# Kernel tuning notes

Measured on AMD Instinct MI355X. Metric: run time of the kernel, lower is better.

Reference implementation:

```python
import jax, jax.numpy as jnp
import numpy as np
import math

V, TB, C, H, L = 50257, 1024, 1024, 16, 8
B, T = 2, 1024
D = C // H


def setup_inputs() -> dict:
    key = jax.random.key(0)
    ks = jax.random.split(key, 16)
    s = 0.02
    n = lambda k, shp: (jax.random.normal(k, shp, jnp.float32) * s)
    inp = {
        "idx": jax.random.randint(ks[0], (B, T), 0, V),
        "tok_emb": n(ks[1], (V, C)),
        "pos_emb": n(ks[2], (1, TB, C)),
        # per-layer stacked params (torch Linear convention: W is [out, in])
        "Wq": n(ks[3], (L, C, C)), "bq": jnp.zeros((L, C)),
        "Wk": n(ks[4], (L, C, C)), "bk": jnp.zeros((L, C)),
        "Wv": n(ks[5], (L, C, C)), "bv": jnp.zeros((L, C)),
        "Wp": n(ks[6], (L, C, C)), "bp": jnp.zeros((L, C)),
        "ln1_w": jnp.ones((L, C)), "ln1_b": jnp.zeros((L, C)),
        "ln2_w": jnp.ones((L, C)), "ln2_b": jnp.zeros((L, C)),
        "W1": n(ks[7], (L, 4 * C, C)), "b1": jnp.zeros((L, 4 * C)),
        "W2": n(ks[8], (L, C, 4 * C)), "b2": jnp.zeros((L, C)),
        "lnf_w": jnp.ones((C,)), "lnf_b": jnp.zeros((C,)),
        "head_w": n(ks[9], (V, C)),
    }
    return inp


def _layer_norm(x, w, b, eps=1e-5):
    mu = x.mean(-1, keepdims=True)
    var = x.var(-1, keepdims=True)
    return (x - mu) * jax.lax.rsqrt(var + eps) * w + b


def _gpt_forward(idx, tok_emb, pos_emb, Wq, bq, Wk, bk, Wv, bv, Wp, bp,
                 ln1_w, ln1_b, ln2_w, ln2_b, W1, b1, W2, b2, lnf_w, lnf_b, head_w):
    b, t = idx.shape
    x = tok_emb[idx] + pos_emb[:, :t, :]  # [B, T, C]; drop = identity (eval)
    causal = jnp.tril(jnp.ones((t, t), dtype=bool))  # [T, T]
    scale = 1.0 / math.sqrt(D)

    def block(x, p):
        (wq, bq_, wk, bk_, wv, bv_, wp, bp_, l1w, l1b, l2w, l2b, w1, b1_, w2, b2_) = p
        h = _layer_norm(x, l1w, l1b)
        q = (h @ wq.T + bq_).reshape(b, t, H, D).transpose(0, 2, 1, 3)  # [B,H,T,D]
        k = (h @ wk.T + bk_).reshape(b, t, H, D).transpose(0, 2, 1, 3)
        v = (h @ wv.T + bv_).reshape(b, t, H, D).transpose(0, 2, 1, 3)
        att = jnp.einsum("bhqd,bhkd->bhqk", q, k) * scale
        att = jnp.where(causal, att, -jnp.inf)
        att = jax.nn.softmax(att, axis=-1)
        y = jnp.einsum("bhqk,bhkd->bhqd", att, v)
        y = y.transpose(0, 2, 1, 3).reshape(b, t, C)
        x = x + (y @ wp.T + bp_)
        h2 = _layer_norm(x, l2w, l2b)
        m = jax.nn.gelu(h2 @ w1.T + b1_, approximate=False)  # torch nn.GELU (erf)
        x = x + (m @ w2.T + b2_)
        return x, None

    params = (Wq, bq, Wk, bk, Wv, bv, Wp, bp, ln1_w, ln1_b, ln2_w, ln2_b, W1, b1, W2, b2)
    x, _ = jax.lax.scan(block, x, params)
    x = _layer_norm(x, lnf_w, lnf_b)
    logits = x @ head_w.T  # [B, T, V]
    return logits


def reference(idx, tok_emb, pos_emb, Wq, bq, Wk, bk, Wv, bv, Wp, bp,
              ln1_w, ln1_b, ln2_w, ln2_b, W1, b1, W2, b2, lnf_w, lnf_b, head_w):
    return _gpt_forward(idx, tok_emb, pos_emb, Wq, bq, Wk, bk, Wv, bv, Wp, bp,
                        ln1_w, ln1_b, ln2_w, ln2_b, W1, b1, W2, b2, lnf_w, lnf_b, head_w)
```

## Files before the change

kernel.cpp:

```cpp
#include <hip/hip_runtime.h>
#include <math.h>

#define V_ 50257
#define C_ 1024
#define H_ 16
#define L_ 8
#define B_ 2
#define T_ 1024
#define BT_ 2048
#define CC_ (C_*C_)
#define QLD_ 3072

typedef unsigned short ushort_t;
using bf16x8 = __attribute__((ext_vector_type(8))) short;
using f32x4  = __attribute__((ext_vector_type(4))) float;

#define AS1 __attribute__((address_space(1)))
#define AS3 __attribute__((address_space(3)))
#define VMCNT0() asm volatile("s_waitcnt vmcnt(0)" ::: "memory")
#define LGKM0()  asm volatile("s_waitcnt lgkmcnt(0)" ::: "memory")
#define RBAR()   asm volatile("s_barrier" ::: "memory")

__device__ __forceinline__ ushort_t f2bf(float f){
  union { float f; unsigned u; } a; a.f = f;
  unsigned r = a.u + 0x7fffu + ((a.u >> 16) & 1u);
  return (ushort_t)(r >> 16);
}

__device__ __forceinline__ unsigned cvtpk_bf16(float a, float b){
  unsigned r;
  asm("v_cvt_pk_bf16_f32 %0, %1, %2" : "=v"(r) : "v"(a), "v"(b));
  return r;
}

__device__ __forceinline__ float wave_sum(float v){
  #pragma unroll
  for(int o=32;o>0;o>>=1) v += __shfl_down(v,o,64);
  return v;
}

__global__ __launch_bounds__(256) void cvt_blk(const float* __restrict__ s, ushort_t* __restrict__ d,
    long inner4, int nblk, long dstStride4){
  long total = inner4 * nblk;
  for(long i = (long)blockIdx.x*256 + threadIdx.x; i < total; i += (long)gridDim.x*256){
    long blk = i / inner4, r = i - blk*inner4;
    float4 v = ((const float4*)s)[i];
    ushort4 o; o.x=f2bf(v.x); o.y=f2bf(v.y); o.z=f2bf(v.z); o.w=f2bf(v.w);
    ((ushort4*)d)[blk*dstStride4 + r] = o;
  }
}

__global__ __launch_bounds__(256) void cvt_qkv(const float* __restrict__ wq,
    const float* __restrict__ wk, const float* __restrict__ wv, ushort_t* __restrict__ d){
  const long inner4 = (long)CC_/4;
  const long total = (long)L_*3*inner4;
  for(long i = (long)blockIdx.x*256 + threadIdx.x; i < total; i += (long)gridDim.x*256){
    long l = i / (3*inner4), r = i - l*3*inner4;
    int which = (int)(r / inner4);
    long rr = r - (long)which*inner4;
    const float* s = (which==0 ? wq : which==1 ? wk : wv) + (l*inner4 + rr)*4;
    float4 v = *(const float4*)s;
    ushort4 o; o.x=f2bf(v.x); o.y=f2bf(v.y); o.z=f2bf(v.z); o.w=f2bf(v.w);
    ((ushort4*)d)[i] = o;
  }
}

__global__ __launch_bounds__(256) void pack_qkv_bias(const float* __restrict__ bq,
    const float* __restrict__ bk, const float* __restrict__ bv, float* __restrict__ dst){
  int i = blockIdx.x*256 + threadIdx.x;
  int l = i / QLD_, c = i - l*QLD_;
  float v;
  if(c < C_)            v = bq[l*C_ + c];
  else if(c < 2*C_)     v = bk[l*C_ + c - C_];
  else                  v = bv[l*C_ + c - 2*C_];
  dst[i] = v;
}

__global__ __launch_bounds__(256) void embed_kernel(const int* __restrict__ idx,
    const float* __restrict__ tok, const float* __restrict__ pos, float* __restrict__ x){
  int i = blockIdx.x*256 + threadIdx.x;
  int c = i & (C_-1); int bt = i >> 10; int t = bt & (T_-1);
  x[i] = tok[(size_t)idx[bt]*C_ + c] + pos[t*C_ + c];
}

__global__ __launch_bounds__(256) void ln_kernel(const float* in, const float* __restrict__ w,
    const float* __restrict__ b, float* outF, ushort_t* outB){
  int row = blockIdx.x;
  const float* xr = in + (size_t)row*C_;
  float vals[4]; float sum=0.f, sq=0.f;
  #pragma unroll
  for(int l=0;l<4;l++){ float v = xr[threadIdx.x + l*256]; vals[l]=v; sum+=v; sq+=v*v; }
  __shared__ float r1[4], r2[4];
  float s1 = wave_sum(sum), s2 = wave_sum(sq);
  int wid = threadIdx.x>>6, lane = threadIdx.x&63;
  if(lane==0){ r1[wid]=s1; r2[wid]=s2; }
  __syncthreads();
  float tot  = r1[0]+r1[1]+r1[2]+r1[3];
  float tot2 = r2[0]+r2[1]+r2[2]+r2[3];
  float mu  = tot * (1.f/C_);
  float var = tot2 * (1.f/C_) - mu*mu;
  float inv = rsqrtf(var + 1e-5f);
  #pragma unroll
  for(int l=0;l<4;l++){
    int c = threadIdx.x + l*256;
    float v = (vals[l]-mu)*inv*w[c] + b[c];
    if(outB) outB[(size_t)row*C_ + c] = f2bf(v);
    else     outF[(size_t)row*C_ + c] = v;
  }
}

template<int BN>
__global__ __launch_bounds__(256) void gemm_mfma(
    const ushort_t* __restrict__ A, const ushort_t* __restrict__ W,
    const float* __restrict__ bias, const float* resid,
    float* outF, ushort_t* outB,
    int M, int N, int K, int act, int nt, int qs)
{
  constexpr int BM = 128;
  constexpr int NSB = BN/16;
  constexpr int NBF = BN/32;
  __shared__ __align__(16) short sA[3][8*512];
  __shared__ __align__(16) short sB[3][NSB*512];
  const int tid  = threadIdx.x;
  const int lane = tid & 63, wid = tid >> 6;
  const int wr = wid >> 1, wc = wid & 1;
  const int nwg = gridDim.x * gridDim.y;
  const int lid = blockIdx.x + gridDim.x * blockIdx.y;
  const int swz = (lid & 7) * (nwg >> 3) + (lid >> 3);
  const int m0 = (swz % gridDim.x) * BM, n0 = (swz / gridDim.x) * BN;
  const int r16 = lane & 15, kq = lane >> 4;

  auto stage = [&](int buf, int k0){
    #pragma unroll
    for(int s2=0; s2<2; ++s2){
      int s = wid*2 + s2;
      const ushort_t* g = A + (size_t)(m0 + s*16 + r16)*K + k0 + kq*8;
      __builtin_amdgcn_global_load_lds((const AS1 void*)g,
          (AS3 void*)&sA[buf][s*512], 16, 0, 0);
    }
    #pragma unroll
    for(int s2=0; s2<NSB/4; ++s2){
      int s = wid*(NSB/4) + s2;
      int gn = n0 + s*16 + r16; if(gn >= N) gn = N-1;
      const ushort_t* g = W + (size_t)gn*K + k0 + kq*8;
      __builtin_amdgcn_global_load_lds((const AS1 void*)g,
          (AS3 void*)&sB[buf][s*512], 16, 0, 0);
    }
  };

  f32x4 acc[4][NBF];
  #pragma unroll
  for(int i=0;i<4;i++)
    #pragma unroll
    for(int j=0;j<NBF;j++) acc[i][j] = (f32x4){0.f,0.f,0.f,0.f};

  const int NT = K >> 5;
  stage(0, 0); stage(1, 32); stage(2, 64);

  int cur = 0;
  for(int t=0; t<NT; ++t){
    if(t+2 < NT){
      if constexpr(BN==128) asm volatile("s_waitcnt vmcnt(8)" ::: "memory");
      else                  asm volatile("s_waitcnt vmcnt(6)" ::: "memory");
    } else if(t+1 < NT){
      if constexpr(BN==128) asm volatile("s_waitcnt vmcnt(4)" ::: "memory");
      else                  asm volatile("s_waitcnt vmcnt(3)" ::: "memory");
    } else {
      VMCNT0();
    }
    RBAR();
    bf16x8 af[4], bfr[NBF];
    #pragma unroll
    for(int m=0;m<4;m++) af[m] = *(const bf16x8*)&sA[cur][(wr*4+m)*512 + lane*8];
    #pragma unroll
    for(int n=0;n<NBF;n++) bfr[n] = *(const bf16x8*)&sB[cur][(wc*NBF+n)*512 + lane*8];
    LGKM0();
    RBAR();
    if(t+3 < NT) stage(cur, (t+3)*32);
    #pragma unroll
    for(int m=0;m<4;m++)
      #pragma unroll
      for(int n=0;n<NBF;n++)
        acc[m][n] = __builtin_amdgcn_mfma_f32_16x16x32_bf16(af[m], bfr[n], acc[m][n], 0, 0, 0);
    cur = (cur==2) ? 0 : cur+1;
  }

  const int colb = n0 + wc*(BN/2);
  #pragma unroll
  for(int m=0;m<4;m++){
    int rowb = m0 + wr*64 + m*16 + kq*4;
    #pragma unroll
    for(int n=0;n<NBF;n++){
      int col = colb + n*16 + r16;
      if(col >= N) continue;
      float bv = bias ? bias[col] : 0.f;
      #pragma unroll
      for(int i=0;i<4;i++){
        int row = rowb + i;
        float v = acc[m][n][i] + bv;
        if(qs && col < C_) v *= 0.125f;
        if(act) v = 0.5f*v*(1.f + erff(v*0.70710678118654752f));
        if(resid) v += resid[(size_t)row*N + col];
        if(outB) outB[(size_t)row*N + col] = f2bf(v);
        else if(nt) __builtin_nontemporal_store(v, &outF[(size_t)row*N + col]);
        else outF[(size_t)row*N + col] = v;
      }
    }
  }
}

template<int BN>
__global__ __launch_bounds__(256) void gemm_s64(
    const ushort_t* __restrict__ A, const ushort_t* __restrict__ W,
    const float* __restrict__ bias, const float* resid,
    float* outF, ushort_t* outB,
    int M, int N, int K, int act, int qs)
{
  constexpr int NSB = BN/16;
  constexpr int NBF = BN/32;
  constexpr int LPW = 1 + NSB/4;
  __shared__ __align__(16) short sA[3][4*512];
  __shared__ __align__(16) short sB[3][NSB*512];
  const int tid  = threadIdx.x;
  const int lane = tid & 63, wid = tid >> 6;
  const int wr = wid >> 1, wc = wid & 1;
  const int nwg = gridDim.x * gridDim.y;
  const int lid = blockIdx.x + gridDim.x * blockIdx.y;
  const int swz = (lid & 7) * (nwg >> 3) + (lid >> 3);
  const int m0 = (swz % gridDim.x) * 64, n0 = (swz / gridDim.x) * BN;
  const int r16 = lane & 15, kq = lane >> 4;

  auto stage = [&](int buf, int k0){
    {
      const ushort_t* g = A + (size_t)(m0 + wid*16 + r16)*K + k0 + kq*8;
      __builtin_amdgcn_global_load_lds((const AS1 void*)g,
          (AS3 void*)&sA[buf][wid*512], 16, 0, 0);
    }
    #pragma unroll
    for(int s2=0; s2<NSB/4; ++s2){
      int s = wid*(NSB/4) + s2;
      const ushort_t* g = W + (size_t)(n0 + s*16 + r16)*K + k0 + kq*8;
      __builtin_amdgcn_global_load_lds((const AS1 void*)g,
          (AS3 void*)&sB[buf][s*512], 16, 0, 0);
    }
  };

  f32x4 acc[2][NBF];
  #pragma unroll
  for(int i=0;i<2;i++)
    #pragma unroll
    for(int j=0;j<NBF;j++) acc[i][j] = (f32x4){0.f,0.f,0.f,0.f};

  const int NT = K >> 5;
  stage(0, 0); stage(1, 32); stage(2, 64);

  int cur = 0;
  for(int t=0; t<NT; ++t){
    if(t+2 < NT){
      if constexpr(LPW==2) asm volatile("s_waitcnt vmcnt(4)" ::: "memory");
      else                 asm volatile("s_waitcnt vmcnt(6)" ::: "memory");
    } else if(t+1 < NT){
      if constexpr(LPW==2) asm volatile("s_waitcnt vmcnt(2)" ::: "memory");
      else                 asm volatile("s_waitcnt vmcnt(3)" ::: "memory");
    } else {
      VMCNT0();
    }
    RBAR();
    bf16x8 af[2], bfr[NBF];
    #pragma unroll
    for(int m=0;m<2;m++) af[m] = *(const bf16x8*)&sA[cur][(wr*2+m)*512 + lane*8];
    #pragma unroll
    for(int n=0;n<NBF;n++) bfr[n] = *(const bf16x8*)&sB[cur][(wc*NBF+n)*512 + lane*8];
    LGKM0();
    RBAR();
    if(t+3 < NT) stage(cur, (t+3)*32);
    #pragma unroll
    for(int m=0;m<2;m++)
      #pragma unroll
      for(int n=0;n<NBF;n++)
        acc[m][n] = __builtin_amdgcn_mfma_f32_16x16x32_bf16(af[m], bfr[n], acc[m][n], 0, 0, 0);
    cur = (cur==2) ? 0 : cur+1;
  }

  const int colb = n0 + wc*(BN/2);
  #pragma unroll
  for(int m=0;m<2;m++){
    int rowb = m0 + wr*32 + m*16 + kq*4;
    #pragma unroll
    for(int n=0;n<NBF;n++){
      int col = colb + n*16 + r16;
      float bv = bias ? bias[col] : 0.f;
      #pragma unroll
      for(int i=0;i<4;i++){
        int row = rowb + i;
        float v = acc[m][n][i] + bv;
        if(qs && col < C_) v *= 0.125f;
        if(act) v = 0.5f*v*(1.f + erff(v*0.70710678118654752f));
        if(resid) v += resid[(size_t)row*N + col];
        if(outB) outB[(size_t)row*N + col] = f2bf(v);
        else outF[(size_t)row*N + col] = v;
      }
    }
  }
}

__global__ __launch_bounds__(256) void flash_kernel(const ushort_t* __restrict__ qkv,
    ushort_t* __restrict__ y){
  const int tid = threadIdx.x, lane = tid & 63, wid = tid >> 6;
  const int r16 = lane & 15, kq = lane >> 4;
  const int lid = blockIdx.x + 16*blockIdx.y;
  const int swz = (lid & 7)*64 + (lid >> 3);
  const int qt = 15 - (swz & 15), bh = swz >> 4;
  const int b = bh >> 4, h = bh & 15;
  const int q0 = qt*64, qw0 = q0 + wid*16;
  const int qa = qw0 + r16;

  __shared__ __align__(16) short Kt[2][8][512];
  __shared__ __align__(16) short VT[2][64][72];
  __shared__ __align__(16) short Pl[4][16][72];
  __shared__ __align__(16) short Ol[4][16][72];

  const size_t rowQ = (size_t)(b*T_ + qa)*QLD_ + h*64 + kq*8;
  bf16x8 qf0 = *(const bf16x8*)(qkv + rowQ);
  bf16x8 qf1 = *(const bf16x8*)(qkv + rowQ + 32);

  auto stageK = [&](int buf, int jt){
    #pragma unroll
    for(int s2=0;s2<2;s2++){
      int s = wid*2 + s2;
      const ushort_t* g = qkv + (size_t)(b*T_ + jt*64 + (s>>1)*16 + r16)*QLD_
                          + C_ + h*64 + (s&1)*32 + kq*8;
      __builtin_amdgcn_global_load_lds((const AS1 void*)g,
          (AS3 void*)&Kt[buf][s][lane*8], 16, 0, 0);
    }
  };

  f32x4 acc[4];
  #pragma unroll
  for(int t=0;t<4;t++) acc[t] = (f32x4){0.f,0.f,0.f,0.f};
  float m_r = -INFINITY, l_r = 0.f;

  {
    stageK(0, 0);
    const ushort_t* vg = qkv + (size_t)(b*T_ + lane)*QLD_ + 2*C_ + h*64;
    bf16x8 va = *(const bf16x8*)(vg + wid*8);
    bf16x8 vb = *(const bf16x8*)(vg + 32 + wid*8);
    VMCNT0();
    #pragma unroll
    for(int j=0;j<8;j++){ VT[0][wid*8+j][lane]=va[j]; VT[0][32+wid*8+j][lane]=vb[j]; }
    __syncthreads();
  }

  const int njt = qt + 1;
  for(int jt=0; jt<njt; ++jt){
    const int cur = jt & 1;
    const bool more = (jt+1) < njt;
    bf16x8 vr0, vr1;
    if(more){
      stageK(cur^1, jt+1);
      const ushort_t* vg = qkv + (size_t)(b*T_ + (jt+1)*64 + lane)*QLD_ + 2*C_ + h*64;
      vr0 = *(const bf16x8*)(vg + wid*8);
      vr1 = *(const bf16x8*)(vg + 32 + wid*8);
    }

    f32x4 st[4];
    __builtin_amdgcn_s_setprio(1);
    #pragma unroll
    for(int kr=0;kr<4;kr++){
      st[kr] = (f32x4){0.f,0.f,0.f,0.f};
      st[kr] = __builtin_amdgcn_mfma_f32_16x16x32_bf16(*(const bf16x8*)&Kt[cur][kr*2+0][lane*8], qf0, st[kr], 0,0,0);
      st[kr] = __builtin_amdgcn_mfma_f32_16x16x32_bf16(*(const bf16x8*)&Kt[cur][kr*2+1][lane*8], qf1, st[kr], 0,0,0);
    }
    __builtin_amdgcn_s_setprio(0);

    float vals[16];
    if(jt == njt-1){
      #pragma unroll
      for(int kr=0;kr<4;kr++)
        #pragma unroll
        for(int i=0;i<4;i++){
          int ka = jt*64 + kr*16 + 4*kq + i;
          vals[kr*4+i] = (ka <= qa) ? st[kr][i] : -INFINITY;
        }
    } else {
      #pragma unroll
      for(int kr=0;kr<4;kr++)
        #pragma unroll
        for(int i=0;i<4;i++) vals[kr*4+i] = st[kr][i];
    }
    float t8[8];
    #pragma unroll
    for(int i=0;i<8;i++) t8[i] = fmaxf(vals[i], vals[i+8]);
    float t4a = fmaxf(t8[0],t8[4]), t4b = fmaxf(t8[1],t8[5]);
    float t4c = fmaxf(t8[2],t8[6]), t4d = fmaxf(t8[3],t8[7]);
    float pmax = fmaxf(fmaxf(t4a,t4b), fmaxf(t4c,t4d));
    pmax = fmaxf(pmax, __shfl_xor(pmax, 16, 64));
    pmax = fmaxf(pmax, __shfl_xor(pmax, 32, 64));

    if(!__all(pmax - m_r <= 8.f)){
      float mnew = fmaxf(m_r, pmax);
      float alpha = __expf(m_r - mnew);
      l_r *= alpha;
      #pragma unroll
      for(int t=0;t<4;t++)
        #pragma unroll
        for(int j=0;j<4;j++) acc[t][j] *= alpha;
      m_r = mnew;
    }

    float ps = 0.f;
    #pragma unroll
    for(int kr=0;kr<4;kr++){
      float p0 = __expf(vals[kr*4+0]-m_r), p1 = __expf(vals[kr*4+1]-m_r);
      float p2 = __expf(vals[kr*4+2]-m_r), p3 = __expf(vals[kr*4+3]-m_r);
      ps += (p0+p1)+(p2+p3);
      *(unsigned*)&Pl[wid][r16][kr*16 + 4*kq]     = cvtpk_bf16(p0, p1);
      *(unsigned*)&Pl[wid][r16][kr*16 + 4*kq + 2] = cvtpk_bf16(p2, p3);
    }
    ps += __shfl_xor(ps, 16, 64);
    ps += __shfl_xor(ps, 32, 64);
    l_r += ps;

    union { bf16x8 v8; uint2 u2[2]; } pf, vf;
    __builtin_amdgcn_s_setprio(1);
    #pragma unroll
    for(int ks2=0; ks2<2; ks2++){
      pf.u2[0] = *(const uint2*)&Pl[wid][r16][ks2*32 + kq*8];
      pf.u2[1] = *(const uint2*)&Pl[wid][r16][ks2*32 + kq*8 + 4];
      #pragma unroll
      for(int db=0; db<4; db++){
        vf.u2[0] = *(const uint2*)&VT[cur][16*db + r16][ks2*32 + kq*8];
        vf.u2[1] = *(const uint2*)&VT[cur][16*db + r16][ks2*32 + kq*8 + 4];
        acc[db] = __builtin_amdgcn_mfma_f32_16x16x32_bf16(vf.v8, pf.v8, acc[db], 0,0,0);
      }
    }
    __builtin_amdgcn_s_setprio(0);

    if(more){
      VMCNT0();
      #pragma unroll
      for(int j=0;j<8;j++){ VT[cur^1][wid*8+j][lane]=vr0[j]; VT[cur^1][32+wid*8+j][lane]=vr1[j]; }
    }
    __syncthreads();
  }

  float linv = 1.f / l_r;
  #pragma unroll
  for(int db=0; db<4; db++)
    #pragma unroll
    for(int i=0;i<4;i++)
      Ol[wid][r16][16*db + 4*kq + i] = (short)f2bf(acc[db][i]*linv);
  int q = lane >> 2, c0 = (lane & 3)*16;
  const short* src = &Ol[wid][q][c0];
  uint2 a0 = *(const uint2*)(src+0), a1 = *(const uint2*)(src+4);
  uint2 a2 = *(const uint2*)(src+8), a3 = *(const uint2*)(src+12);
  ushort_t* dst = y + (size_t)(b*T_ + qw0 + q)*C_ + h*64 + c0;
  uint4 w0 = {a0.x, a0.y, a1.x, a1.y}, w1 = {a2.x, a2.y, a3.x, a3.y};
  *(uint4*)(dst+0) = w0;
  *(uint4*)(dst+8) = w1;
}

__global__ __launch_bounds__(256) void gemm_nt(const float* __restrict__ A, const float* __restrict__ W,
    const float* __restrict__ bias, const float* resid, float* Cm,
    int M, int N, int K, int act){
  __shared__ float As[16][68];
  __shared__ float Bs[16][68];
  int m0 = blockIdx.y*64, n0 = blockIdx.x*64;
  int tid = threadIdx.x;
  int tx = tid & 15, ty = tid >> 4;
  float acc[4][4] = {};
  for(int k0=0;k0<K;k0+=16){
    #pragma unroll
    for(int l=0;l<4;l++){
      int li = tid + l*256;
      int r = li >> 4, c = li & 15;
      int gm = m0 + r, gn = n0 + r, gk = k0 + c;
      As[c][r] = (gm<M) ? A[(size_t)gm*K + gk] : 0.f;
      Bs[c][r] = (gn<N) ? W[(size_t)gn*K + gk] : 0.f;
    }
    __syncthreads();
    #pragma unroll
    for(int k=0;k<16;k++){
      float4 av = *(const float4*)&As[k][ty*4];
      float4 bv = *(const float4*)&Bs[k][tx*4];
      float a[4] = {av.x, av.y, av.z, av.w};
      float b4[4] = {bv.x, bv.y, bv.z, bv.w};
      #pragma unroll
      for(int i=0;i<4;i++)
        #pragma unroll
        for(int j=0;j<4;j++)
          acc[i][j] = fmaf(a[i], b4[j], acc[i][j]);
    }
    __syncthreads();
  }
  #pragma unroll
  for(int i=0;i<4;i++){
    int m = m0 + ty*4 + i; if(m>=M) continue;
    #pragma unroll
    for(int j=0;j<4;j++){
      int n = n0 + tx*4 + j; if(n>=N) continue;
      float v = acc[i][j];
      if(bias) v += bias[n];
      if(act)  v = 0.5f*v*(1.f + erff(v*0.70710678118654752f));
      if(resid) v += resid[(size_t)m*N + n];
      Cm[(size_t)m*N + n] = v;
    }
  }
}

extern "C" void kernel_launch(void* const* d_in, const int* in_sizes, int n_in,
                              void* d_out, int out_size, void* d_ws, size_t ws_size,
                              hipStream_t stream) {
  const int*   idx  = (const int*)  d_in[0];
  const float* tok  = (const float*)d_in[1];
  const float* pos  = (const float*)d_in[2];
  const float* Wq   = (const float*)d_in[3];
  const float* bq   = (const float*)d_in[4];
  const float* Wk   = (const float*)d_in[5];
  const float* bk   = (const float*)d_in[6];
  const float* Wv   = (const float*)d_in[7];
  const float* bv   = (const float*)d_in[8];
  const float* Wp   = (const float*)d_in[9];
  const float* bp   = (const float*)d_in[10];
  const float* ln1w = (const float*)d_in[11];
  const float* ln1b = (const float*)d_in[12];
  const float* ln2w = (const float*)d_in[13];
  const float* ln2b = (const float*)d_in[14];
  const float* W1   = (const float*)d_in[15];
  const float* b1   = (const float*)d_in[16];
  const float* W2   = (const float*)d_in[17];
  const float* b2   = (const float*)d_in[18];
  const float* lnfw = (const float*)d_in[19];
  const float* lnfb = (const float*)d_in[20];
  const float* headw= (const float*)d_in[21];

  float* out = (float*)d_out;
  ushort_t* qkvb = (ushort_t*)(out);
  ushort_t* hb   = (ushort_t*)(out + 3145728);
  ushort_t* yb   = (ushort_t*)(out + 4194304);
  ushort_t* mb   = (ushort_t*)(out + 5242880);
  ushort_t* wqkv = (ushort_t*)(out + 9437184);
  ushort_t* wpb  = (ushort_t*)(out + 22020096);
  ushort_t* w1b  = (ushort_t*)(out + 26214400);
  ushort_t* w2b  = (ushort_t*)(out + 42991616);
  float*    bqkv = out + 59768832;
  float*    x    = (float*)d_ws;
  ushort_t* xb   = (ushort_t*)((float*)d_ws + 2097152);
  ushort_t* whb  = (ushort_t*)((float*)d_ws + 3145728);
  const bool big = ws_size >= (size_t)28877312 * 4;

  cvt_qkv<<<4096,256,0,stream>>>(Wq, Wk, Wv, wqkv);
  cvt_blk<<<2048,256,0,stream>>>(Wp, wpb,  (long)L_*CC_/4,   1, (long)L_*CC_/4);
  cvt_blk<<<2048,256,0,stream>>>(W1, w1b,  (long)L_*CC_,     1, (long)L_*CC_);
  cvt_blk<<<2048,256,0,stream>>>(W2, w2b,  (long)L_*CC_,     1, (long)L_*CC_);
  if(big) cvt_blk<<<2048,256,0,stream>>>(headw, whb, (long)V_*C_/4, 1, (long)V_*C_/4);
  pack_qkv_bias<<<L_*QLD_/256,256,0,stream>>>(bq, bk, bv, bqkv);

  embed_kernel<<<BT_*C_/256, 256, 0, stream>>>(idx, tok, pos, x);

  for(int l=0;l<L_;l++){
    ln_kernel<<<BT_,256,0,stream>>>(x, ln1w + l*C_, ln1b + l*C_, nullptr, hb);
    gemm_s64<128><<<dim3(BT_/64, QLD_/128),256,0,stream>>>(hb, wqkv + (size_t)l*3*CC_,
        bqkv + l*QLD_, nullptr, nullptr, qkvb, BT_, QLD_, C_, 0, 1);
    flash_kernel<<<dim3(T_/64, B_*H_),256,0,stream>>>(qkvb, yb);
    gemm_s64<64><<<dim3(BT_/64, C_/64),256,0,stream>>>(yb, wpb + (size_t)l*CC_,
        bp + l*C_, x, x, nullptr, BT_, C_, C_, 0, 0);
    ln_kernel<<<BT_,256,0,stream>>>(x, ln2w + l*C_, ln2b + l*C_, nullptr, hb);
    gemm_s64<128><<<dim3(BT_/64, 4*C_/128),256,0,stream>>>(hb, w1b + (size_t)l*4*CC_,
        b1 + (size_t)l*4*C_, nullptr, nullptr, mb, BT_, 4*C_, C_, 1, 0);
    gemm_s64<64><<<dim3(BT_/64, C_/64),256,0,stream>>>(mb, w2b + (size_t)l*4*CC_,
        b2 + l*C_, x, x, nullptr, BT_, C_, 4*C_, 0, 0);
  }

  if(big){
    ln_kernel<<<BT_,256,0,stream>>>(x, lnfw, lnfb, nullptr, xb);
    gemm_mfma<128><<<dim3(BT_/128, (V_+127)/128),256,0,stream>>>(xb, whb,
        nullptr, nullptr, out, nullptr, BT_, V_, C_, 0, 1, 0);
  } else {
    ln_kernel<<<BT_,256,0,stream>>>(x, lnfw, lnfb, x, nullptr);
    gemm_nt<<<dim3((V_+63)/64, BT_/64),256,0,stream>>>(x, headw, nullptr, nullptr, out,
                                                       BT_, V_, C_, 0);
  }
}
```

Baseline: 2.667 ms.

## Fuse weight conversions, deepen head GEMM pipeline, add K64 GEMM for projections

Merges the separate fp32-to-bf16 weight conversion launches into one kernel, which cuts launch overhead. Moves the large head GEMM to a 4-stage LDS pipeline with matching vmcnt waits, so more loads are in flight while MFMAs run. Adds a new 64x64 GEMM that stages K=64 per iteration, with fewer barriers per unit of K, and uses it for the attention-output and MLP-down projections. The costs are extra LDS per block, which may lower occupancy, and a combined conversion kernel with branchy indexing.

```diff
diff --git a/kernel.cpp b/kernel.cpp
--- a/kernel.cpp
+++ b/kernel.cpp
@@ -39,29 +39,34 @@
   return v;
 }
 
-__global__ __launch_bounds__(256) void cvt_blk(const float* __restrict__ s, ushort_t* __restrict__ d,
-    long inner4, int nblk, long dstStride4){
-  long total = inner4 * nblk;
-  for(long i = (long)blockIdx.x*256 + threadIdx.x; i < total; i += (long)gridDim.x*256){
-    long blk = i / inner4, r = i - blk*inner4;
-    float4 v = ((const float4*)s)[i];
-    ushort4 o; o.x=f2bf(v.x); o.y=f2bf(v.y); o.z=f2bf(v.z); o.w=f2bf(v.w);
-    ((ushort4*)d)[blk*dstStride4 + r] = o;
-  }
-}
-
-__global__ __launch_bounds__(256) void cvt_qkv(const float* __restrict__ wq,
-    const float* __restrict__ wk, const float* __restrict__ wv, ushort_t* __restrict__ d){
+__global__ __launch_bounds__(256) void cvt_all(
+    const float* __restrict__ wq, const float* __restrict__ wk, const float* __restrict__ wv,
+    const float* __restrict__ wp, const float* __restrict__ w1, const float* __restrict__ w2,
+    const float* __restrict__ wh,
+    ushort_t* __restrict__ dqkv, ushort_t* __restrict__ dp, ushort_t* __restrict__ d1,
+    ushort_t* __restrict__ d2, ushort_t* __restrict__ dh, long n5)
+{
   const long inner4 = (long)CC_/4;
-  const long total = (long)L_*3*inner4;
-  for(long i = (long)blockIdx.x*256 + threadIdx.x; i < total; i += (long)gridDim.x*256){
-    long l = i / (3*inner4), r = i - l*3*inner4;
-    int which = (int)(r / inner4);
-    long rr = r - (long)which*inner4;
-    const float* s = (which==0 ? wq : which==1 ? wk : wv) + (l*inner4 + rr)*4;
+  const long n1 = (long)L_*3*inner4;
+  const long n2 = (long)L_*inner4;
+  const long n3 = (long)L_*4*inner4;
+  const long n4 = n3;
+  const long c1 = n1, c2 = c1+n2, c3 = c2+n3, c4 = c3+n4, c5 = c4+n5;
+  for(long i = (long)blockIdx.x*256 + threadIdx.x; i < c5; i += (long)gridDim.x*256){
+    const float* s; ushort_t* d; long di;
+    if(i < c1){
+      long l = i / (3*inner4), r = i - l*3*inner4;
+      int which = (int)(r / inner4);
+      long rr = r - (long)which*inner4;
+      s = (which==0 ? wq : which==1 ? wk : wv) + (l*inner4 + rr)*4;
+      d = dqkv; di = i;
+    } else if(i < c2){ long j = i-c1; s = wp + j*4; d = dp; di = j; }
+    else if(i < c3){ long j = i-c2; s = w1 + j*4; d = d1; di = j; }
+    else if(i < c4){ long j = i-c3; s = w2 + j*4; d = d2; di = j; }
+    else           { long j = i-c4; s = wh + j*4; d = dh; di = j; }
     float4 v = *(const float4*)s;
     ushort4 o; o.x=f2bf(v.x); o.y=f2bf(v.y); o.z=f2bf(v.z); o.w=f2bf(v.w);
-    ((ushort4*)d)[i] = o;
+    ((ushort4*)d)[di] = o;
   }
 }
 
@@ -119,8 +124,8 @@
   constexpr int BM = 128;
   constexpr int NSB = BN/16;
   constexpr int NBF = BN/32;
-  __shared__ __align__(16) short sA[3][8*512];
-  __shared__ __align__(16) short sB[3][NSB*512];
+  __shared__ __align__(16) short sA[4][8*512];
+  __shared__ __align__(16) short sB[4][NSB*512];
   const int tid  = threadIdx.x;
   const int lane = tid & 63, wid = tid >> 6;
   const int wr = wid >> 1, wc = wid & 1;
@@ -155,11 +160,14 @@
     for(int j=0;j<NBF;j++) acc[i][j] = (f32x4){0.f,0.f,0.f,0.f};
 
   const int NT = K >> 5;
-  stage(0, 0); stage(1, 32); stage(2, 64);
+  stage(0, 0); stage(1, 32); stage(2, 64); stage(3, 96);
 
   int cur = 0;
   for(int t=0; t<NT; ++t){
-    if(t+2 < NT){
+    if(t+3 < NT){
+      if constexpr(BN==128) asm volatile("s_waitcnt vmcnt(12)" ::: "memory");
+      else                  asm volatile("s_waitcnt vmcnt(9)"  ::: "memory");
+    } else if(t+2 < NT){
       if constexpr(BN==128) asm volatile("s_waitcnt vmcnt(8)" ::: "memory");
       else                  asm volatile("s_waitcnt vmcnt(6)" ::: "memory");
     } else if(t+1 < NT){
@@ -176,13 +184,13 @@
     for(int n=0;n<NBF;n++) bfr[n] = *(const bf16x8*)&sB[cur][(wc*NBF+n)*512 + lane*8];
     LGKM0();
     RBAR();
-    if(t+3 < NT) stage(cur, (t+3)*32);
+    if(t+4 < NT) stage(cur, (t+4)*32);
     #pragma unroll
     for(int m=0;m<4;m++)
       #pragma unroll
       for(int n=0;n<NBF;n++)
         acc[m][n] = __builtin_amdgcn_mfma_f32_16x16x32_bf16(af[m], bfr[n], acc[m][n], 0, 0, 0);
-    cur = (cur==2) ? 0 : cur+1;
+    cur = (cur+1) & 3;
   }
 
   const int colb = n0 + wc*(BN/2);
@@ -296,6 +304,90 @@
         float v = acc[m][n][i] + bv;
         if(qs && col < C_) v *= 0.125f;
         if(act) v = 0.5f*v*(1.f + erff(v*0.70710678118654752f));
+        if(resid) v += resid[(size_t)row*N + col];
+        if(outB) outB[(size_t)row*N + col] = f2bf(v);
+        else outF[(size_t)row*N + col] = v;
+      }
+    }
+  }
+}
+
+__global__ __launch_bounds__(256) void gemm_s64k64(
+    const ushort_t* __restrict__ A, const ushort_t* __restrict__ W,
+    const float* __restrict__ bias, const float* resid,
+    float* outF, ushort_t* outB,
+    int M, int N, int K)
+{
+  __shared__ __align__(16) short sA[3][2][4*512];
+  __shared__ __align__(16) short sB[3][2][4*512];
+  const int tid  = threadIdx.x;
+  const int lane = tid & 63, wid = tid >> 6;
+  const int wr = wid >> 1, wc = wid & 1;
+  const int nwg = gridDim.x * gridDim.y;
+  const int lid = blockIdx.x + gridDim.x * blockIdx.y;
+  const int swz = (lid & 7) * (nwg >> 3) + (lid >> 3);
+  const int m0 = (swz % gridDim.x) * 64, n0 = (swz / gridDim.x) * 64;
+  const int r16 = lane & 15, kq = lane >> 4;
+
+  auto stage = [&](int buf, int k0){
+    #pragma unroll
+    for(int h=0; h<2; ++h){
+      const ushort_t* ga = A + (size_t)(m0 + wid*16 + r16)*K + k0 + h*32 + kq*8;
+      __builtin_amdgcn_global_load_lds((const AS1 void*)ga,
+          (AS3 void*)&sA[buf][h][wid*512], 16, 0, 0);
+      const ushort_t* gb = W + (size_t)(n0 + wid*16 + r16)*K + k0 + h*32 + kq*8;
+      __builtin_amdgcn_global_load_lds((const AS1 void*)gb,
+          (AS3 void*)&sB[buf][h][wid*512], 16, 0, 0);
+    }
+  };
+
+  f32x4 acc[2][2];
+  #pragma unroll
+  for(int i=0;i<2;i++)
+    #pragma unroll
+    for(int j=0;j<2;j++) acc[i][j] = (f32x4){0.f,0.f,0.f,0.f};
+
+  const int NT = K >> 6;
+  stage(0, 0); stage(1, 64); stage(2, 128);
+
+  int cur = 0;
+  for(int t=0; t<NT; ++t){
+    if(t+2 < NT)      asm volatile("s_waitcnt vmcnt(8)" ::: "memory");
+    else if(t+1 < NT) asm volatile("s_waitcnt vmcnt(4)" ::: "memory");
+    else              VMCNT0();
+    RBAR();
+    bf16x8 af[2][2], bfr[2][2];
+    #pragma unroll
+    for(int ks=0; ks<2; ++ks){
+      #pragma unroll
+      for(int m=0;m<2;m++) af[ks][m] = *(const bf16x8*)&sA[cur][ks][(wr*2+m)*512 + lane*8];
+      #pragma unroll
+      for(int n=0;n<2;n++) bfr[ks][n] = *(const bf16x8*)&sB[cur][ks][(wc*2+n)*512 + lane*8];
+    }
+    LGKM0();
+    RBAR();
+    if(t+3 < NT) stage(cur, (t+3)*64);
+    #pragma unroll
+    for(int ks=0; ks<2; ++ks)
+      #pragma unroll
+      for(int m=0;m<2;m++)
+        #pragma unroll
+        for(int n=0;n<2;n++)
+          acc[m][n] = __builtin_amdgcn_mfma_f32_16x16x32_bf16(af[ks][m], bfr[ks][n], acc[m][n], 0, 0, 0);
+    cur = (cur==2) ? 0 : cur+1;
+  }
+
+  #pragma unroll
+  for(int m=0;m<2;m++){
+    int rowb = m0 + wr*32 + m*16 + kq*4;
+    #pragma unroll
+    for(int n=0;n<2;n++){
+      int col = n0 + wc*32 + n*16 + r16;
+      float bv = bias ? bias[col] : 0.f;
+      #pragma unroll
+      for(int i=0;i<4;i++){
+        int row = rowb + i;
+        float v = acc[m][n][i] + bv;
         if(resid) v += resid[(size_t)row*N + col];
         if(outB) outB[(size_t)row*N + col] = f2bf(v);
         else outF[(size_t)row*N + col] = v;
@@ -549,11 +641,8 @@
   ushort_t* whb  = (ushort_t*)((float*)d_ws + 3145728);
   const bool big = ws_size >= (size_t)28877312 * 4;
 
-  cvt_qkv<<<4096,256,0,stream>>>(Wq, Wk, Wv, wqkv);
-  cvt_blk<<<2048,256,0,stream>>>(Wp, wpb,  (long)L_*CC_/4,   1, (long)L_*CC_/4);
-  cvt_blk<<<2048,256,0,stream>>>(W1, w1b,  (long)L_*CC_,     1, (long)L_*CC_);
-  cvt_blk<<<2048,256,0,stream>>>(W2, w2b,  (long)L_*CC_,     1, (long)L_*CC_);
-  if(big) cvt_blk<<<2048,256,0,stream>>>(headw, whb, (long)V_*C_/4, 1, (long)V_*C_/4);
+  cvt_all<<<4096,256,0,stream>>>(Wq, Wk, Wv, Wp, W1, W2, headw,
+      wqkv, wpb, w1b, w2b, whb, big ? (long)V_*C_/4 : 0);
   pack_qkv_bias<<<L_*QLD_/256,256,0,stream>>>(bq, bk, bv, bqkv);
 
   embed_kernel<<<BT_*C_/256, 256, 0, stream>>>(idx, tok, pos, x);
@@ -563,13 +652,13 @@
     gemm_s64<128><<<dim3(BT_/64, QLD_/128),256,0,stream>>>(hb, wqkv + (size_t)l*3*CC_,
         bqkv + l*QLD_, nullptr, nullptr, qkvb, BT_, QLD_, C_, 0, 1);
     flash_kernel<<<dim3(T_/64, B_*H_),256,0,stream>>>(qkvb, yb);
-    gemm_s64<64><<<dim3(BT_/64, C_/64),256,0,stream>>>(yb, wpb + (size_t)l*CC_,
-        bp + l*C_, x, x, nullptr, BT_, C_, C_, 0, 0);
+    gemm_s64k64<<<dim3(BT_/64, C_/64),256,0,stream>>>(yb, wpb + (size_t)l*CC_,
+        bp + l*C_, x, x, nullptr, BT_, C_, C_);
     ln_kernel<<<BT_,256,0,stream>>>(x, ln2w + l*C_, ln2b + l*C_, nullptr, hb);
     gemm_s64<128><<<dim3(BT_/64, 4*C_/128),256,0,stream>>>(hb, w1b + (size_t)l*4*CC_,
         b1 + (size_t)l*4*C_, nullptr, nullptr, mb, BT_, 4*C_, C_, 1, 0);
-    gemm_s64<64><<<dim3(BT_/64, C_/64),256,0,stream>>>(mb, w2b + (size_t)l*4*CC_,
-        b2 + l*C_, x, x, nullptr, BT_, C_, 4*C_, 0, 0);
+    gemm_s64k64<<<dim3(BT_/64, C_/64),256,0,stream>>>(mb, w2b + (size_t)l*4*CC_,
+        b2 + l*C_, x, x, nullptr, BT_, C_, 4*C_);
   }
 
   if(big){
```

After: 2.651 ms. Within noise of the previous version (-0.6%).
